# Kernel optimization log

Measured on AMD Instinct MI355X. Metric: run time of the kernel, lower is better.

## Reference

```python
import jax, jax.numpy as jnp
import numpy as np

ALPHA = 1.702
EPS_RMS = 1e-6
W_LOAD = 0.01
W_IMP = 0.01
W_AUX = 1.0
LIMIT = 7.0
K_TOP = 4


def swiglu(x, alpha=ALPHA, limit=LIMIT):
    x_glu = jnp.clip(x[..., ::2], -limit, limit)
    x_lin = jnp.clip(x[..., 1::2], -limit, limit)
    return x_glu * jax.nn.sigmoid(x_glu * alpha) + (x_lin + 1.0)


def setup_inputs() -> dict:
    key = jax.random.key(0)
    ks = jax.random.split(key, 4)
    T, H, I, E = 2048, 512, 512, 8
    x = jax.random.normal(ks[0], (T, H), dtype=jnp.float32)
    norm_scale = jnp.ones((H,), jnp.float32)
    gate_w = jax.random.normal(ks[1], (E, H), jnp.float32) * 0.02
    gate_b = jnp.zeros((E,), jnp.float32)
    mlp1_w = jax.random.normal(ks[2], (E, 2 * I, H), jnp.float32) * 0.02
    mlp1_b = jnp.zeros((E, 2 * I), jnp.float32)
    mlp2_w = jax.random.normal(ks[3], (E, H, I), jnp.float32) * 0.02
    mlp2_b = jnp.zeros((E, H), jnp.float32)
    return {"x": x, "norm_scale": norm_scale, "gate_w": gate_w, "gate_b": gate_b,
            "mlp1_w": mlp1_w, "mlp1_b": mlp1_b, "mlp2_w": mlp2_w, "mlp2_b": mlp2_b}


def reference(x, norm_scale, gate_w, gate_b, mlp1_w, mlp1_b, mlp2_w, mlp2_b):
    T, H = x.shape
    E = gate_w.shape[0]
    K = K_TOP
    # RMSNorm (fp32 math as in torch module)
    t = x * jax.lax.rsqrt(jnp.mean(x * x, axis=-1, keepdims=True) + EPS_RMS) * norm_scale
    # gating
    gate_logits = t @ gate_w.T + gate_b                      # [T, E]
    gate_probs = jax.nn.softmax(gate_logits, axis=-1)
    expert_weights, experts_indices = jax.lax.top_k(gate_probs, K)
    expert_weights = expert_weights / expert_weights.sum(axis=-1, keepdims=True)
    # per-token per-expert combine coefficient (sum of slot weights routed to e)
    coeff = jnp.zeros((T, E), x.dtype).at[jnp.arange(T)[:, None], experts_indices].add(expert_weights)
    # dense expert compute (math-equivalent to the gathered einsums; avoids
    # materializing per-token weight matrices)
    h = jnp.einsum('th,ech->tec', t, mlp1_w) + mlp1_b[None]  # [T, E, 2I]
    a = swiglu(h)                                            # [T, E, I]
    y = jnp.einsum('tei,ehi->teh', a, mlp2_w) + mlp2_b[None] # [T, E, H]
    out = jnp.einsum('teh,te->th', y, coeff) + x
    # aux losses (replicates the torch code exactly, incl. D-doubling quirk)
    P = gate_probs.mean(axis=0)                              # [E]
    counts = jax.vmap(lambda col: jnp.zeros((E,), x.dtype).at[col].add(1.0), in_axes=1)(experts_indices)  # [K, E]
    doubling = (2.0 ** (K - jnp.arange(K))).astype(x.dtype)  # D_i = 2*(D_{i-1}+c_i)
    D = (doubling[:, None] * counts).sum(axis=0) / (T * K)
    loss_load = W_LOAD * E * (P * D).sum()
    importance = gate_logits.sum(axis=0)
    cv = jnp.std(importance, ddof=1) / (importance.mean() + 1e-6)
    loss_imp = W_IMP * cv ** 2
    aux_loss = W_AUX * (loss_load + loss_imp)
    return out, aux_loss
```

## Files before the change

### kernel.cpp

```cpp
#include <hip/hip_runtime.h>
#include <stdint.h>

#define ALPHA 1.702f
#define LIMIT 7.0f

typedef float f32x4 __attribute__((ext_vector_type(4)));
typedef __bf16 bf16x8 __attribute__((ext_vector_type(8)));

static __device__ __forceinline__ unsigned short f2bf(float f) {
    union { float f; uint32_t u; } v; v.f = f;
    uint32_t u = v.u;
    return (unsigned short)((u + 0x7FFFu + ((u >> 16) & 1u)) >> 16);
}

#define GLL16(GP, LP) __builtin_amdgcn_global_load_lds( \
    (const __attribute__((address_space(1))) void*)(GP), \
    (__attribute__((address_space(3))) void*)(LP), 16, 0, 0)

static __device__ __forceinline__ int lsw(int row, int kc) {
    return row * 4 + (kc ^ ((row >> 1) & 3));
}

__global__ __launch_bounds__(256) void prep_kernel(
    const float* __restrict__ w1, const float* __restrict__ w2,
    unsigned short* __restrict__ w1p, unsigned short* __restrict__ w2b,
    const float* __restrict__ x,
    const float* __restrict__ norm_scale,
    const float* __restrict__ gate_w,
    const float* __restrict__ gate_b,
    const float* __restrict__ b2,
    unsigned short* __restrict__ t_bf,
    float* __restrict__ coeff,
    float* __restrict__ paux,
    float* __restrict__ out)
{
    __shared__ float red[4][48];
    if (blockIdx.x < 6144) {
        const int idx = blockIdx.x * 256 + threadIdx.x;
        const int n1 = 1048576;
        if (idx < n1) {
            const int e = idx >> 17;
            const int rem = idx & 131071;
            const int r = rem >> 7;
            const int c = rem & 127;
            const int src = (r < 512) ? (2 * r) : (2 * (r - 512) + 1);
            float4 v = ((const float4*)w1)[(e << 17) + (src << 7) + c];
            ushort4 o = { f2bf(v.x), f2bf(v.y), f2bf(v.z), f2bf(v.w) };
            ((ushort4*)w1p)[idx] = o;
        } else {
            const int i2 = idx - n1;
            float4 v = ((const float4*)w2)[i2];
            ushort4 o = { f2bf(v.x), f2bf(v.y), f2bf(v.z), f2bf(v.w) };
            ((ushort4*)w2b)[i2] = o;
        }
        return;
    }
    const int bid = blockIdx.x - 6144;
    const int wave = threadIdx.x >> 6;
    const int lane = threadIdx.x & 63;

    float accP[8], accI[8], accC[32];
    #pragma unroll
    for (int e = 0; e < 8; ++e) { accP[e] = 0.f; accI[e] = 0.f; }
    #pragma unroll
    for (int i = 0; i < 32; ++i) accC[i] = 0.f;

    #pragma unroll
    for (int it = 0; it < 2; ++it) {
        const int t = bid * 8 + wave * 2 + it;
        const float4* xr = (const float4*)(x + t * 512);
        float4 x0 = xr[lane * 2];
        float4 x1 = xr[lane * 2 + 1];
        float ss = x0.x*x0.x + x0.y*x0.y + x0.z*x0.z + x0.w*x0.w
                 + x1.x*x1.x + x1.y*x1.y + x1.z*x1.z + x1.w*x1.w;
        #pragma unroll
        for (int off = 32; off > 0; off >>= 1) ss += __shfl_xor(ss, off, 64);
        const float rstd = rsqrtf(ss * (1.f / 512.f) + 1e-6f);
        const float4* sr = (const float4*)norm_scale;
        float4 s0 = sr[lane * 2], s1 = sr[lane * 2 + 1];
        float tv[8];
        tv[0] = x0.x * rstd * s0.x; tv[1] = x0.y * rstd * s0.y;
        tv[2] = x0.z * rstd * s0.z; tv[3] = x0.w * rstd * s0.w;
        tv[4] = x1.x * rstd * s1.x; tv[5] = x1.y * rstd * s1.y;
        tv[6] = x1.z * rstd * s1.z; tv[7] = x1.w * rstd * s1.w;
        uint32_t p0 = (uint32_t)f2bf(tv[0]) | ((uint32_t)f2bf(tv[1]) << 16);
        uint32_t p1 = (uint32_t)f2bf(tv[2]) | ((uint32_t)f2bf(tv[3]) << 16);
        uint32_t p2 = (uint32_t)f2bf(tv[4]) | ((uint32_t)f2bf(tv[5]) << 16);
        uint32_t p3 = (uint32_t)f2bf(tv[6]) | ((uint32_t)f2bf(tv[7]) << 16);
        uint4 pk; pk.x = p0; pk.y = p1; pk.z = p2; pk.w = p3;
        ((uint4*)(t_bf + t * 512))[lane] = pk;
        float le[8];
        #pragma unroll
        for (int e = 0; e < 8; ++e) {
            const float4* gw = (const float4*)(gate_w + e * 512);
            float4 g0 = gw[lane * 2], g1 = gw[lane * 2 + 1];
            float d = tv[0]*g0.x + tv[1]*g0.y + tv[2]*g0.z + tv[3]*g0.w
                    + tv[4]*g1.x + tv[5]*g1.y + tv[6]*g1.z + tv[7]*g1.w;
            #pragma unroll
            for (int off = 32; off > 0; off >>= 1) d += __shfl_xor(d, off, 64);
            le[e] = d + gate_b[e];
        }
        float mx = le[0];
        #pragma unroll
        for (int e = 1; e < 8; ++e) mx = fmaxf(mx, le[e]);
        float pe[8], se = 0.f;
        #pragma unroll
        for (int e = 0; e < 8; ++e) { pe[e] = __expf(le[e] - mx); se += pe[e]; }
        const float sinv = 1.f / se;
        #pragma unroll
        for (int e = 0; e < 8; ++e) pe[e] *= sinv;
        unsigned picked = 0;
        int ik[4]; float wk[4];
        #pragma unroll
        for (int k = 0; k < 4; ++k) {
            float bv = -1.f; int bi = 0;
            #pragma unroll
            for (int e = 0; e < 8; ++e)
                if (!(picked & (1u << e)) && pe[e] > bv) { bv = pe[e]; bi = e; }
            ik[k] = bi; wk[k] = bv; picked |= (1u << bi);
        }
        const float winv = 1.f / (wk[0] + wk[1] + wk[2] + wk[3]);
        float nw[4];
        #pragma unroll
        for (int k = 0; k < 4; ++k) nw[k] = wk[k] * winv;
        float ce[8];
        #pragma unroll
        for (int e = 0; e < 8; ++e) {
            float c = 0.f;
            #pragma unroll
            for (int k = 0; k < 4; ++k) c += (ik[k] == e) ? nw[k] : 0.f;
            ce[e] = c;
        }
        if (lane == 0) {
            #pragma unroll
            for (int e = 0; e < 8; ++e) coeff[t * 8 + e] = ce[e];
        }
        #pragma unroll
        for (int e = 0; e < 8; ++e) { accP[e] += pe[e]; accI[e] += le[e]; }
        #pragma unroll
        for (int k = 0; k < 4; ++k)
            #pragma unroll
            for (int e = 0; e < 8; ++e)
                accC[k * 8 + e] += (ik[k] == e) ? 1.f : 0.f;
        float ov[8];
        ov[0] = x0.x; ov[1] = x0.y; ov[2] = x0.z; ov[3] = x0.w;
        ov[4] = x1.x; ov[5] = x1.y; ov[6] = x1.z; ov[7] = x1.w;
        #pragma unroll
        for (int e = 0; e < 8; ++e) {
            const float4* br = (const float4*)(b2 + e * 512);
            float4 b0 = br[lane * 2], bb1 = br[lane * 2 + 1];
            ov[0] += ce[e] * b0.x; ov[1] += ce[e] * b0.y;
            ov[2] += ce[e] * b0.z; ov[3] += ce[e] * b0.w;
            ov[4] += ce[e] * bb1.x; ov[5] += ce[e] * bb1.y;
            ov[6] += ce[e] * bb1.z; ov[7] += ce[e] * bb1.w;
        }
        float4 o0, o1;
        o0.x = ov[0]; o0.y = ov[1]; o0.z = ov[2]; o0.w = ov[3];
        o1.x = ov[4]; o1.y = ov[5]; o1.z = ov[6]; o1.w = ov[7];
        float4* orow = (float4*)(out + t * 512);
        orow[lane * 2] = o0; orow[lane * 2 + 1] = o1;
    }
    if (lane == 0) {
        #pragma unroll
        for (int e = 0; e < 8; ++e) { red[wave][e] = accP[e]; red[wave][8 + e] = accI[e]; }
        #pragma unroll
        for (int i = 0; i < 32; ++i) red[wave][16 + i] = accC[i];
    }
    __syncthreads();
    if (threadIdx.x < 48) {
        paux[bid * 48 + threadIdx.x] =
            red[0][threadIdx.x] + red[1][threadIdx.x]
          + red[2][threadIdx.x] + red[3][threadIdx.x];
    }
}

__global__ __launch_bounds__(256, 2) void gemm1_swiglu(
    const unsigned short* __restrict__ A,
    const unsigned short* __restrict__ w1p,
    const float* __restrict__ b1,
    const float* __restrict__ coeff,
    unsigned short* __restrict__ As,
    const float* __restrict__ paux,
    float* __restrict__ aux_out)
{
    if (blockIdx.x == 512) {
        __shared__ float sred[4][48];
        const int wv = threadIdx.x >> 6, ln = threadIdx.x & 63;
        if (ln < 48) {
            float s = 0.f;
            for (int b = 0; b < 64; ++b) s += paux[(wv * 64 + b) * 48 + ln];
            sred[wv][ln] = s;
        }
        __syncthreads();
        if (threadIdx.x == 0) {
            float imp[8], sl = 0.f;
            #pragma unroll
            for (int e = 0; e < 8; ++e) {
                float a0 = sred[0][e] + sred[1][e] + sred[2][e] + sred[3][e];
                float P = a0 * (1.f / 2048.f);
                imp[e] = sred[0][8+e] + sred[1][8+e] + sred[2][8+e] + sred[3][8+e];
                float c0 = sred[0][16+e] + sred[1][16+e] + sred[2][16+e] + sred[3][16+e];
                float c1 = sred[0][24+e] + sred[1][24+e] + sred[2][24+e] + sred[3][24+e];
                float c2 = sred[0][32+e] + sred[1][32+e] + sred[2][32+e] + sred[3][32+e];
                float c3 = sred[0][40+e] + sred[1][40+e] + sred[2][40+e] + sred[3][40+e];
                float D = (16.f * c0 + 8.f * c1 + 4.f * c2 + 2.f * c3) * (1.f / 8192.f);
                sl += P * D;
            }
            float loss_load = 0.01f * 8.f * sl;
            float mean = 0.f;
            #pragma unroll
            for (int e = 0; e < 8; ++e) mean += imp[e];
            mean *= 0.125f;
            float var = 0.f;
            #pragma unroll
            for (int e = 0; e < 8; ++e) { float d = imp[e] - mean; var += d * d; }
            var *= (1.f / 7.f);
            float cv = sqrtf(var) / (mean + 1e-6f);
            *aux_out = loss_load + 0.01f * cv * cv;
        }
        return;
    }
    __shared__ unsigned short tA[2][4096];
    __shared__ unsigned short tBg[2][4096];
    __shared__ unsigned short tBl[2][4096];
    const int tid = threadIdx.x;
    const int bx = blockIdx.x;
    const int xcd = bx & 7;
    const int slot = bx >> 3;
    const int tile_m = slot >> 2;
    const int g = xcd * 4 + (slot & 3);
    const int e = g >> 2;
    const int np = (g & 3) * 128;
    const int m0 = tile_m * 128;
    const int lane = tid & 63, wave = tid >> 6;
    const int wm = (wave & 1) * 64, wn = (wave >> 1) * 64;
    const int quad = lane >> 4, l16 = lane & 15;
    const int srow = tid >> 2;
    const int soff = ((tid & 3) ^ ((tid >> 3) & 3)) * 8;

    const unsigned short* Ar0 = A + (m0 + srow) * 512 + soff;
    const unsigned short* Ar1 = A + (m0 + 64 + srow) * 512 + soff;
    const unsigned short* Bg = w1p + (e * 1024 + np) * 512;
    const unsigned short* Bg0 = Bg + srow * 512 + soff;
    const unsigned short* Bg1 = Bg + (64 + srow) * 512 + soff;
    const unsigned short* Bl0 = Bg0 + 512 * 512;
    const unsigned short* Bl1 = Bg1 + 512 * 512;

    int rA[4], rB[4];
    #pragma unroll
    for (int i = 0; i < 4; ++i) {
        rA[i] = lsw(wm + i * 16 + l16, quad) * 8;
        rB[i] = lsw(wn + i * 16 + l16, quad) * 8;
    }

    f32x4 accG[4][4], accL[4][4];
    #pragma unroll
    for (int i = 0; i < 4; ++i)
        #pragma unroll
        for (int j = 0; j < 4; ++j) {
            f32x4 z = {0.f, 0.f, 0.f, 0.f};
            accG[i][j] = z; accL[i][j] = z;
        }

#define STAGE1(s, k0) do { \
    GLL16(Ar0 + (k0), tA[s] + tid * 8); \
    GLL16(Ar1 + (k0), tA[s] + (tid + 256) * 8); \
    GLL16(Bg0 + (k0), tBg[s] + tid * 8); \
    GLL16(Bg1 + (k0), tBg[s] + (tid + 256) * 8); \
    GLL16(Bl0 + (k0), tBl[s] + tid * 8); \
    GLL16(Bl1 + (k0), tBl[s] + (tid + 256) * 8); \
} while (0)

    STAGE1(0, 0);
    STAGE1(1, 32);
    #pragma unroll
    for (int kt = 0; kt < 16; ++kt) {
        const int cur = kt & 1;
        if (kt < 15) asm volatile("s_waitcnt vmcnt(6)" ::: "memory");
        else         asm volatile("s_waitcnt vmcnt(0)" ::: "memory");
        asm volatile("s_barrier" ::: "memory");
        bf16x8 af[4], bg[4], bl[4];
        #pragma unroll
        for (int i = 0; i < 4; ++i) {
            af[i] = *(const bf16x8*)(tA[cur] + rA[i]);
            bg[i] = *(const bf16x8*)(tBg[cur] + rB[i]);
            bl[i] = *(const bf16x8*)(tBl[cur] + rB[i]);
        }
        asm volatile("s_waitcnt lgkmcnt(0)" ::: "memory");
        asm volatile("s_barrier" ::: "memory");
        if (kt < 14) STAGE1(cur, (kt + 2) * 32);
        #pragma unroll
        for (int i = 0; i < 4; ++i)
            #pragma unroll
            for (int j = 0; j < 4; ++j) {
                accG[i][j] = __builtin_amdgcn_mfma_f32_16x16x32_bf16(af[i], bg[j], accG[i][j], 0, 0, 0);
                accL[i][j] = __builtin_amdgcn_mfma_f32_16x16x32_bf16(af[i], bl[j], accL[i][j], 0, 0, 0);
            }
    }
#undef STAGE1

    float cw[4][4];
    #pragma unroll
    for (int i = 0; i < 4; ++i) {
        const int rowb = m0 + wm + i * 16 + quad * 4;
        #pragma unroll
        for (int r = 0; r < 4; ++r) cw[i][r] = coeff[(rowb + r) * 8 + e];
    }
    #pragma unroll
    for (int j = 0; j < 4; ++j) {
        const int colp = np + wn + j * 16 + l16;
        const float bgv = b1[e * 1024 + 2 * colp];
        const float blv = b1[e * 1024 + 2 * colp + 1];
        #pragma unroll
        for (int i = 0; i < 4; ++i) {
            const int rowb = m0 + wm + i * 16 + quad * 4;
            #pragma unroll
            for (int r = 0; r < 4; ++r) {
                float g2 = fminf(fmaxf(accG[i][j][r] + bgv, -LIMIT), LIMIT);
                float l2 = fminf(fmaxf(accL[i][j][r] + blv, -LIMIT), LIMIT);
                float a = g2 / (1.f + __expf(-ALPHA * g2)) + l2 + 1.f;
                a *= cw[i][r];
                As[(rowb + r) * 4096 + e * 512 + colp] = f2bf(a);
            }
        }
    }
}

__global__ __launch_bounds__(256, 2) void gemm2(
    const unsigned short* __restrict__ As,
    const unsigned short* __restrict__ w2b,
    float* __restrict__ out)
{
    __shared__ unsigned short tA[2][4096];
    __shared__ unsigned short tB[2][4096];
    const int tid = threadIdx.x;
    const int bx = blockIdx.x;
    const int e = bx & 7;
    const int slot = bx >> 3;
    const int tile_m = slot >> 2;
    const int tile_n = slot & 3;
    const int m0 = tile_m * 128, n0 = tile_n * 128;
    const int lane = tid & 63, wave = tid >> 6;
    const int wm = (wave & 1) * 64, wn = (wave >> 1) * 64;
    const int quad = lane >> 4, l16 = lane & 15;
    const int srow = tid >> 2;
    const int soff = ((tid & 3) ^ ((tid >> 3) & 3)) * 8;

    const unsigned short* Ar0 = As + (m0 + srow) * 4096 + e * 512 + soff;
    const unsigned short* Ar1 = As + (m0 + 64 + srow) * 4096 + e * 512 + soff;
    const unsigned short* Bb  = w2b + e * 262144;
    const unsigned short* Br0 = Bb + (n0 + srow) * 512 + soff;
    const unsigned short* Br1 = Bb + (n0 + 64 + srow) * 512 + soff;

    int rA[4], rB[4];
    #pragma unroll
    for (int i = 0; i < 4; ++i) {
        rA[i] = lsw(wm + i * 16 + l16, quad) * 8;
        rB[i] = lsw(wn + i * 16 + l16, quad) * 8;
    }

    f32x4 acc[4][4];
    #pragma unroll
    for (int i = 0; i < 4; ++i)
        #pragma unroll
        for (int j = 0; j < 4; ++j) { f32x4 z = {0.f, 0.f, 0.f, 0.f}; acc[i][j] = z; }

#define STAGE2(s, k0) do { \
    GLL16(Ar0 + (k0), tA[s] + tid * 8); \
    GLL16(Ar1 + (k0), tA[s] + (tid + 256) * 8); \
    GLL16(Br0 + (k0), tB[s] + tid * 8); \
    GLL16(Br1 + (k0), tB[s] + (tid + 256) * 8); \
} while (0)

    STAGE2(0, 0);
    STAGE2(1, 32);
    #pragma unroll
    for (int kt = 0; kt < 16; ++kt) {
        const int cur = kt & 1;
        if (kt < 15) asm volatile("s_waitcnt vmcnt(4)" ::: "memory");
        else         asm volatile("s_waitcnt vmcnt(0)" ::: "memory");
        asm volatile("s_barrier" ::: "memory");
        bf16x8 af[4], bf[4];
        #pragma unroll
        for (int i = 0; i < 4; ++i) {
            af[i] = *(const bf16x8*)(tA[cur] + rA[i]);
            bf[i] = *(const bf16x8*)(tB[cur] + rB[i]);
        }
        asm volatile("s_waitcnt lgkmcnt(0)" ::: "memory");
        asm volatile("s_barrier" ::: "memory");
        if (kt < 14) STAGE2(cur, (kt + 2) * 32);
        #pragma unroll
        for (int i = 0; i < 4; ++i)
            #pragma unroll
            for (int j = 0; j < 4; ++j)
                acc[i][j] = __builtin_amdgcn_mfma_f32_16x16x32_bf16(af[i], bf[j], acc[i][j], 0, 0, 0);
    }
#undef STAGE2

    #pragma unroll
    for (int j = 0; j < 4; ++j) {
        const int col = n0 + wn + j * 16 + l16;
        #pragma unroll
        for (int i = 0; i < 4; ++i) {
            const int rowb = m0 + wm + i * 16 + quad * 4;
            #pragma unroll
            for (int r = 0; r < 4; ++r)
                atomicAdd(&out[(rowb + r) * 512 + col], acc[i][j][r]);
        }
    }
}

extern "C" void kernel_launch(void* const* d_in, const int* in_sizes, int n_in,
                              void* d_out, int out_size, void* d_ws, size_t ws_size,
                              hipStream_t stream)
{
    (void)in_sizes; (void)n_in; (void)out_size; (void)ws_size;
    const float* x          = (const float*)d_in[0];
    const float* norm_scale = (const float*)d_in[1];
    const float* gate_w     = (const float*)d_in[2];
    const float* gate_b     = (const float*)d_in[3];
    const float* mlp1_w     = (const float*)d_in[4];
    const float* mlp1_b     = (const float*)d_in[5];
    const float* mlp2_w     = (const float*)d_in[6];
    const float* mlp2_b     = (const float*)d_in[7];
    float* out = (float*)d_out;

    char* ws = (char*)d_ws;
    unsigned short* w1p   = (unsigned short*)(ws);
    unsigned short* w2b   = (unsigned short*)(ws + 8388608);
    unsigned short* tbf   = (unsigned short*)(ws + 12582912);
    unsigned short* As    = (unsigned short*)(ws + 14680064);
    float*          coeff = (float*)(ws + 31457280);
    float*          paux  = (float*)(ws + 31522816);

    prep_kernel<<<6400, 256, 0, stream>>>(mlp1_w, mlp2_w, w1p, w2b,
                                          x, norm_scale, gate_w, gate_b, mlp2_b,
                                          tbf, coeff, paux, out);
    gemm1_swiglu<<<513, 256, 0, stream>>>(tbf, w1p, mlp1_b, coeff, As,
                                          paux, out + 2048 * 512);
    gemm2<<<512, 256, 0, stream>>>(As, w2b, out);
}
```

Before: 158.6 us.

## Route tokens to experts sparsely instead of dense all-expert GEMMs

Prep now builds per-expert token lists and weights, using shared-memory atomics and then global atomic counters. Both GEMMs gather the routed tokens for each expert and exit tiles that lie past the expert's count, so only the top-4 of 8 experts are computed per token instead of all 8. The cost is gathered A-row loads, bounds checks, scattered atomic adds into the output, and a memset of the counters. Expert load is data-dependent and can be unbalanced, but the grid stays sized for the worst case.

```diff
diff --git a/kernel.cpp b/kernel.cpp
--- a/kernel.cpp
+++ b/kernel.cpp
@@ -12,6 +12,7 @@
     uint32_t u = v.u;
     return (unsigned short)((u + 0x7FFFu + ((u >> 16) & 1u)) >> 16);
 }
+static __device__ __forceinline__ int imin(int a, int b) { return a < b ? a : b; }
 
 #define GLL16(GP, LP) __builtin_amdgcn_global_load_lds( \
     (const __attribute__((address_space(1))) void*)(GP), \
@@ -30,25 +31,31 @@
     const float* __restrict__ gate_b,
     const float* __restrict__ b2,
     unsigned short* __restrict__ t_bf,
-    float* __restrict__ coeff,
+    int* __restrict__ idx,
+    float* __restrict__ wcoef,
+    int* __restrict__ cnt,
     float* __restrict__ paux,
     float* __restrict__ out)
 {
     __shared__ float red[4][48];
+    __shared__ int   ltok[8][8];
+    __shared__ float lwt[8][8];
+    __shared__ int   lcnt[8];
+    __shared__ int   gbase[8];
     if (blockIdx.x < 6144) {
-        const int idx = blockIdx.x * 256 + threadIdx.x;
+        const int i4 = blockIdx.x * 256 + threadIdx.x;
         const int n1 = 1048576;
-        if (idx < n1) {
-            const int e = idx >> 17;
-            const int rem = idx & 131071;
+        if (i4 < n1) {
+            const int e = i4 >> 17;
+            const int rem = i4 & 131071;
             const int r = rem >> 7;
             const int c = rem & 127;
             const int src = (r < 512) ? (2 * r) : (2 * (r - 512) + 1);
             float4 v = ((const float4*)w1)[(e << 17) + (src << 7) + c];
             ushort4 o = { f2bf(v.x), f2bf(v.y), f2bf(v.z), f2bf(v.w) };
-            ((ushort4*)w1p)[idx] = o;
+            ((ushort4*)w1p)[i4] = o;
         } else {
-            const int i2 = idx - n1;
+            const int i2 = i4 - n1;
             float4 v = ((const float4*)w2)[i2];
             ushort4 o = { f2bf(v.x), f2bf(v.y), f2bf(v.z), f2bf(v.w) };
             ((ushort4*)w2b)[i2] = o;
@@ -58,6 +65,8 @@
     const int bid = blockIdx.x - 6144;
     const int wave = threadIdx.x >> 6;
     const int lane = threadIdx.x & 63;
+    if (threadIdx.x < 8) lcnt[threadIdx.x] = 0;
+    __syncthreads();
 
     float accP[8], accI[8], accC[32];
     #pragma unroll
@@ -133,7 +142,11 @@
         }
         if (lane == 0) {
             #pragma unroll
-            for (int e = 0; e < 8; ++e) coeff[t * 8 + e] = ce[e];
+            for (int k = 0; k < 4; ++k) {
+                const int e = ik[k];
+                const int pos = atomicAdd(&lcnt[e], 1);
+                ltok[e][pos] = t; lwt[e][pos] = nw[k];
+            }
         }
         #pragma unroll
         for (int e = 0; e < 8; ++e) { accP[e] += pe[e]; accI[e] += le[e]; }
@@ -167,6 +180,17 @@
         for (int i = 0; i < 32; ++i) red[wave][16 + i] = accC[i];
     }
     __syncthreads();
+    if (threadIdx.x < 8)
+        gbase[threadIdx.x] = atomicAdd(&cnt[threadIdx.x], lcnt[threadIdx.x]);
+    __syncthreads();
+    if (threadIdx.x < 64) {
+        const int e = threadIdx.x >> 3, i = threadIdx.x & 7;
+        if (i < lcnt[e]) {
+            const int g = gbase[e] + i;
+            idx[e * 2048 + g] = ltok[e][i];
+            wcoef[e * 2048 + g] = lwt[e][i];
+        }
+    }
     if (threadIdx.x < 48) {
         paux[bid * 48 + threadIdx.x] =
             red[0][threadIdx.x] + red[1][threadIdx.x]
@@ -178,7 +202,9 @@
     const unsigned short* __restrict__ A,
     const unsigned short* __restrict__ w1p,
     const float* __restrict__ b1,
-    const float* __restrict__ coeff,
+    const int* __restrict__ idx,
+    const float* __restrict__ wcoef,
+    const int* __restrict__ cnt,
     unsigned short* __restrict__ As,
     const float* __restrict__ paux,
     float* __restrict__ aux_out)
@@ -220,26 +246,28 @@
         }
         return;
     }
+    const int bx = blockIdx.x;
+    const int e = bx & 7;
+    const int slot = bx >> 3;
+    const int tile_m = slot >> 2, tile_n = slot & 3;
+    const int m0 = tile_m * 128, np = tile_n * 128;
+    const int cnte = cnt[e];
+    if (m0 >= cnte) return;
+
     __shared__ unsigned short tA[2][4096];
     __shared__ unsigned short tBg[2][4096];
     __shared__ unsigned short tBl[2][4096];
     const int tid = threadIdx.x;
-    const int bx = blockIdx.x;
-    const int xcd = bx & 7;
-    const int slot = bx >> 3;
-    const int tile_m = slot >> 2;
-    const int g = xcd * 4 + (slot & 3);
-    const int e = g >> 2;
-    const int np = (g & 3) * 128;
-    const int m0 = tile_m * 128;
     const int lane = tid & 63, wave = tid >> 6;
     const int wm = (wave & 1) * 64, wn = (wave >> 1) * 64;
     const int quad = lane >> 4, l16 = lane & 15;
     const int srow = tid >> 2;
     const int soff = ((tid & 3) ^ ((tid >> 3) & 3)) * 8;
 
-    const unsigned short* Ar0 = A + (m0 + srow) * 512 + soff;
-    const unsigned short* Ar1 = A + (m0 + 64 + srow) * 512 + soff;
+    const int tok0 = idx[e * 2048 + imin(m0 + srow, cnte - 1)];
+    const int tok1 = idx[e * 2048 + imin(m0 + 64 + srow, cnte - 1)];
+    const unsigned short* Ar0 = A + tok0 * 512 + soff;
+    const unsigned short* Ar1 = A + tok1 * 512 + soff;
     const unsigned short* Bg = w1p + (e * 1024 + np) * 512;
     const unsigned short* Bg0 = Bg + srow * 512 + soff;
     const unsigned short* Bg1 = Bg + (64 + srow) * 512 + soff;
@@ -299,13 +327,6 @@
     }
 #undef STAGE1
 
-    float cw[4][4];
-    #pragma unroll
-    for (int i = 0; i < 4; ++i) {
-        const int rowb = m0 + wm + i * 16 + quad * 4;
-        #pragma unroll
-        for (int r = 0; r < 4; ++r) cw[i][r] = coeff[(rowb + r) * 8 + e];
-    }
     #pragma unroll
     for (int j = 0; j < 4; ++j) {
         const int colp = np + wn + j * 16 + l16;
@@ -313,14 +334,17 @@
         const float blv = b1[e * 1024 + 2 * colp + 1];
         #pragma unroll
         for (int i = 0; i < 4; ++i) {
-            const int rowb = m0 + wm + i * 16 + quad * 4;
+            const int sb = m0 + wm + i * 16 + quad * 4;
             #pragma unroll
             for (int r = 0; r < 4; ++r) {
-                float g2 = fminf(fmaxf(accG[i][j][r] + bgv, -LIMIT), LIMIT);
-                float l2 = fminf(fmaxf(accL[i][j][r] + blv, -LIMIT), LIMIT);
-                float a = g2 / (1.f + __expf(-ALPHA * g2)) + l2 + 1.f;
-                a *= cw[i][r];
-                As[(rowb + r) * 4096 + e * 512 + colp] = f2bf(a);
+                const int s = sb + r;
+                if (s < cnte) {
+                    float g2 = fminf(fmaxf(accG[i][j][r] + bgv, -LIMIT), LIMIT);
+                    float l2 = fminf(fmaxf(accL[i][j][r] + blv, -LIMIT), LIMIT);
+                    float a = g2 / (1.f + __expf(-ALPHA * g2)) + l2 + 1.f;
+                    a *= wcoef[e * 2048 + s];
+                    As[e * 1048576 + s * 512 + colp] = f2bf(a);
+                }
             }
         }
     }
@@ -329,25 +353,29 @@
 __global__ __launch_bounds__(256, 2) void gemm2(
     const unsigned short* __restrict__ As,
     const unsigned short* __restrict__ w2b,
+    const int* __restrict__ idx,
+    const int* __restrict__ cnt,
     float* __restrict__ out)
 {
+    const int bx = blockIdx.x;
+    const int e = bx & 7;
+    const int slot = bx >> 3;
+    const int tile_m = slot >> 2, tile_n = slot & 3;
+    const int m0 = tile_m * 128, n0 = tile_n * 128;
+    const int cnte = cnt[e];
+    if (m0 >= cnte) return;
+
     __shared__ unsigned short tA[2][4096];
     __shared__ unsigned short tB[2][4096];
     const int tid = threadIdx.x;
-    const int bx = blockIdx.x;
-    const int e = bx & 7;
-    const int slot = bx >> 3;
-    const int tile_m = slot >> 2;
-    const int tile_n = slot & 3;
-    const int m0 = tile_m * 128, n0 = tile_n * 128;
     const int lane = tid & 63, wave = tid >> 6;
     const int wm = (wave & 1) * 64, wn = (wave >> 1) * 64;
     const int quad = lane >> 4, l16 = lane & 15;
     const int srow = tid >> 2;
     const int soff = ((tid & 3) ^ ((tid >> 3) & 3)) * 8;
 
-    const unsigned short* Ar0 = As + (m0 + srow) * 4096 + e * 512 + soff;
-    const unsigned short* Ar1 = As + (m0 + 64 + srow) * 4096 + e * 512 + soff;
+    const unsigned short* Ar0 = As + e * 1048576 + (m0 + srow) * 512 + soff;
+    const unsigned short* Ar1 = As + e * 1048576 + (m0 + 64 + srow) * 512 + soff;
     const unsigned short* Bb  = w2b + e * 262144;
     const unsigned short* Br0 = Bb + (n0 + srow) * 512 + soff;
     const unsigned short* Br1 = Bb + (n0 + 64 + srow) * 512 + soff;
@@ -398,14 +426,19 @@
 #undef STAGE2
 
     #pragma unroll
-    for (int j = 0; j < 4; ++j) {
-        const int col = n0 + wn + j * 16 + l16;
-        #pragma unroll
-        for (int i = 0; i < 4; ++i) {
-            const int rowb = m0 + wm + i * 16 + quad * 4;
-            #pragma unroll
-            for (int r = 0; r < 4; ++r)
-                atomicAdd(&out[(rowb + r) * 512 + col], acc[i][j][r]);
+    for (int i = 0; i < 4; ++i) {
+        const int sb = m0 + wm + i * 16 + quad * 4;
+        #pragma unroll
+        for (int r = 0; r < 4; ++r) {
+            const int s = sb + r;
+            if (s < cnte) {
+                const int tok = idx[e * 2048 + s];
+                #pragma unroll
+                for (int j = 0; j < 4; ++j) {
+                    const int col = n0 + wn + j * 16 + l16;
+                    atomicAdd(&out[tok * 512 + col], acc[i][j][r]);
+                }
+            }
         }
     }
 }
@@ -430,13 +463,16 @@
     unsigned short* w2b   = (unsigned short*)(ws + 8388608);
     unsigned short* tbf   = (unsigned short*)(ws + 12582912);
     unsigned short* As    = (unsigned short*)(ws + 14680064);
-    float*          coeff = (float*)(ws + 31457280);
-    float*          paux  = (float*)(ws + 31522816);
-
+    int*            idx   = (int*)(ws + 31457280);
+    float*          wcoef = (float*)(ws + 31522816);
+    float*          paux  = (float*)(ws + 31588352);
+    int*            cnt   = (int*)(ws + 31637504);
+
+    hipMemsetAsync(cnt, 0, 32, stream);
     prep_kernel<<<6400, 256, 0, stream>>>(mlp1_w, mlp2_w, w1p, w2b,
                                           x, norm_scale, gate_w, gate_b, mlp2_b,
-                                          tbf, coeff, paux, out);
-    gemm1_swiglu<<<513, 256, 0, stream>>>(tbf, w1p, mlp1_b, coeff, As,
-                                          paux, out + 2048 * 512);
-    gemm2<<<512, 256, 0, stream>>>(As, w2b, out);
-}
+                                          tbf, idx, wcoef, cnt, paux, out);
+    gemm1_swiglu<<<513, 256, 0, stream>>>(tbf, w1p, mlp1_b, idx, wcoef, cnt,
+                                          As, paux, out + 2048 * 512);
+    gemm2<<<512, 256, 0, stream>>>(As, w2b, idx, cnt, out);
+}
```

After: 153.1 us. 3.5% less time.
